# Optimization experiments

Measured on AMD Instinct MI355X. Metric: run time of the kernel, lower is better.

Reference implementation:

```python
import jax, jax.numpy as jnp
import numpy as np

B, C, T, H, W = 8, 512, 8, 32, 32
CI = C // 2  # inter_channels
EPS = 1e-5


def _conv1x1(x, w, b):
    # x: (b, c, t, h, w); w: (o, c); b: (o,)
    return jnp.einsum('bcthw,oc->bothw', x, w) + b[None, :, None, None, None]


def _maxpool2(v):
    # MaxPool3d(kernel=2, stride=2) on (t, h, w)
    b, c, t, h, w = v.shape
    return v.reshape(b, c, t // 2, 2, h // 2, 2, w // 2, 2).max(axis=(3, 5, 7))


def setup_inputs() -> dict:
    key = jax.random.key(0)
    ks = jax.random.split(key, 12)
    s = 0.02
    return {
        'x': jax.random.normal(ks[0], (B, C, T, H, W), dtype=jnp.float32),
        'theta_w': jax.random.normal(ks[1], (CI, C), dtype=jnp.float32) * s,
        'theta_b': jnp.zeros((CI,), dtype=jnp.float32),
        'phi_w': jax.random.normal(ks[2], (CI, C), dtype=jnp.float32) * s,
        'phi_b': jnp.zeros((CI,), dtype=jnp.float32),
        'g_w': jax.random.normal(ks[3], (CI, C), dtype=jnp.float32) * s,
        'g_b': jnp.zeros((CI,), dtype=jnp.float32),
        'wz_w': jax.random.normal(ks[4], (C, CI), dtype=jnp.float32) * s,
        'wz_b': jnp.zeros((C,), dtype=jnp.float32),
        'bn_gamma': jax.random.uniform(ks[5], (C,), dtype=jnp.float32, minval=0.5, maxval=1.5),
        'bn_beta': jax.random.normal(ks[6], (C,), dtype=jnp.float32) * 0.1,
    }


def reference(x, theta_w, theta_b, phi_w, phi_b, g_w, g_b, wz_w, wz_b, bn_gamma, bn_beta):
    b = x.shape[0]
    # projections (1x1x1 convs == channel matmuls)
    theta_x = _conv1x1(x, theta_w, theta_b)            # (b, ci, t, h, w)
    phi_x = _maxpool2(_conv1x1(x, phi_w, phi_b))       # (b, ci, t/2, h/2, w/2)
    g_x = _maxpool2(_conv1x1(x, g_w, g_b))             # (b, ci, t/2, h/2, w/2)

    ci = theta_x.shape[1]
    q = theta_x.reshape(b, ci, -1).transpose(0, 2, 1)  # (b, N, ci)
    k = phi_x.reshape(b, ci, -1)                       # (b, ci, M)
    v = g_x.reshape(b, ci, -1).transpose(0, 2, 1)      # (b, M, ci)

    f = jnp.einsum('bnc,bcm->bnm', q, k)               # (b, N, M)
    attn = jax.nn.softmax(f, axis=-1)                  # embedded_gaussian
    y = jnp.einsum('bnm,bmc->bnc', attn, v)            # (b, N, ci)
    y = y.transpose(0, 2, 1).reshape(b, ci, *x.shape[2:])

    # Wz: 1x1x1 conv + BatchNorm3d (training-mode batch stats, eps=1e-5)
    z = _conv1x1(y, wz_w, wz_b)                        # (b, C, t, h, w)
    mean = z.mean(axis=(0, 2, 3, 4), keepdims=True)
    var = z.var(axis=(0, 2, 3, 4), keepdims=True)
    z = (z - mean) * jax.lax.rsqrt(var + EPS)
    z = z * bn_gamma[None, :, None, None, None] + bn_beta[None, :, None, None, None]
    return z + x
```

## Files before the change

kernel.cpp:

```cpp
#include <hip/hip_runtime.h>
#include <math.h>

typedef unsigned short u16;
typedef __attribute__((ext_vector_type(8))) _Float16 half8;
typedef __attribute__((ext_vector_type(4))) float f32x4;

#define NS 8192
#define MS 1024
#define CCH 512
#define CI 256
#define O3 768

__device__ __forceinline__ float h2f(u16 u) {
    _Float16 h; *(u16*)&h = u; return (float)h;
}
__device__ __forceinline__ u16 f2h(float f) {
    _Float16 h = (_Float16)f; return *(u16*)&h;
}

__device__ __forceinline__ void gld16(u16* lds, const u16* g) {
    __builtin_amdgcn_global_load_lds((const __attribute__((address_space(1))) void*)g,
                                     (__attribute__((address_space(3))) void*)lds,
                                     16, 0, 0);
}

template<int CTRL>
__device__ __forceinline__ float dppmax(float x) {
    union { float f; int i; } a, b;
    a.f = x;
    b.i = __builtin_amdgcn_update_dpp(a.i, a.i, CTRL, 0xF, 0xF, false);
    return fmaxf(a.f, b.f);
}
__device__ __forceinline__ float rowmax16(float x) {
    x = dppmax<0xB1>(x);
    x = dppmax<0x4E>(x);
    x = dppmax<0x141>(x);
    x = dppmax<0x140>(x);
    return x;
}

__global__ void prep_w(const float* __restrict__ tw, const float* __restrict__ tb,
                       const float* __restrict__ pw, const float* __restrict__ pb,
                       const float* __restrict__ gw, const float* __restrict__ gb,
                       const float* __restrict__ wzw,
                       u16* __restrict__ W3b, float* __restrict__ b3, u16* __restrict__ wzb) {
    int i = blockIdx.x * 256 + threadIdx.x;
    if (i < O3 * CCH) {
        int o = i >> 9, c = i & 511;
        float v = (o < 256) ? tw[o * 512 + c] : (o < 512) ? pw[(o - 256) * 512 + c]
                                              : gw[(o - 512) * 512 + c];
        W3b[i] = f2h(v);
    } else {
        int j = i - O3 * CCH;
        if (j < CCH * CI) wzb[j] = f2h(wzw[j]);
    }
    if (i < O3) b3[i] = (i < 256) ? tb[i] : (i < 512) ? pb[i - 256] : gb[i - 512];
}

__global__ __launch_bounds__(256) void transpose_x(const float* __restrict__ x,
                                                   u16* __restrict__ xt) {
    __shared__ float tile[64][129];
    int b = blockIdx.z;
    int n0 = blockIdx.x * 128, c0 = blockIdx.y * 64;
    const float* xb = x + ((size_t)b * CCH + c0) * NS + n0;
    int t = threadIdx.x;
    #pragma unroll
    for (int i = 0; i < 32; ++i) {
        int idx = t + i * 256;
        int c = idx >> 7, n = idx & 127;
        tile[c][n] = xb[(size_t)c * NS + n];
    }
    __syncthreads();
    u16* xo = xt + ((size_t)b * NS + n0) * CCH + c0;
    #pragma unroll
    for (int i = 0; i < 16; ++i) {
        int idx = t + i * 256;
        int cp = idx & 31, n = idx >> 5;
        unsigned lo = f2h(tile[2 * cp][n]);
        unsigned hi = f2h(tile[2 * cp + 1][n]);
        *(unsigned*)(xo + (size_t)n * CCH + 2 * cp) = lo | (hi << 16);
    }
}

__global__ __launch_bounds__(256) void proj_gemm(
        const u16* __restrict__ A, const u16* __restrict__ Bm,
        const float* __restrict__ bias,
        u16* __restrict__ projq, u16* __restrict__ P1) {
    __shared__ u16 As[2][128 * 64];
    __shared__ u16 Bs[2][128 * 64];
    const int t = threadIdx.x;
    const int l = t & 63, w = t >> 6;
    const int wr = w >> 1, wc = w & 1;
    const int fr = l & 15, fq = l >> 4;

    const int nx = gridDim.x, ny = gridDim.y;
    int bid = blockIdx.x + nx * (blockIdx.y + ny * blockIdx.z);
    int cpx = (nx * ny * (int)gridDim.z) >> 3;
    int Wd = (bid & 7) * cpx + (bid >> 3);
    int bx = Wd % nx, rem = Wd / nx;
    int by = rem % ny, bz = rem / ny;

    const u16* gA = A + (size_t)bz * NS * CCH + (size_t)(by * 128) * CCH;
    const u16* gB = Bm + (size_t)(bx * 128) * CCH;

    f32x4 acc[4][4];
    #pragma unroll
    for (int m = 0; m < 4; ++m)
        #pragma unroll
        for (int n = 0; n < 4; ++n) acc[m][n] = (f32x4)0.f;

    #define STAGE_AB(buf, k0)                                                 \
        {                                                                     \
            _Pragma("unroll")                                                 \
            for (int i = 0; i < 4; ++i) {                                     \
                int cd = t + i * 256;                                         \
                int row = cd >> 3;                                            \
                int k8 = ((cd & 7) ^ (row & 7)) * 8;                          \
                int lbase = (cd & ~63) * 8;                                   \
                gld16(&As[buf][lbase], gA + (size_t)row * CCH + (k0) + k8);   \
                gld16(&Bs[buf][lbase], gB + (size_t)row * CCH + (k0) + k8);   \
            }                                                                 \
        }

    const int nk = CCH >> 6;
    STAGE_AB(0, 0);
    STAGE_AB(1, 64);

    for (int mt = 0; mt < nk; ++mt) {
        const int cur = mt & 1;
        if (mt == nk - 1) asm volatile("s_waitcnt vmcnt(0)" ::: "memory");
        else              asm volatile("s_waitcnt vmcnt(8)" ::: "memory");
        __builtin_amdgcn_sched_barrier(0);
        __builtin_amdgcn_s_barrier();

        half8 fa[4][2], fb[4][2];
        #pragma unroll
        for (int m = 0; m < 4; ++m)
            #pragma unroll
            for (int kk = 0; kk < 2; ++kk) {
                int ra = wr * 64 + m * 16 + fr;
                int rb = wc * 64 + m * 16 + fr;
                fa[m][kk] = *(const half8*)&As[cur][ra * 64 + ((((kk << 2) | fq)) ^ (ra & 7)) * 8];
                fb[m][kk] = *(const half8*)&Bs[cur][rb * 64 + ((((kk << 2) | fq)) ^ (rb & 7)) * 8];
            }
        __builtin_amdgcn_s_setprio(1);
        #pragma unroll
        for (int kk = 0; kk < 2; ++kk)
            #pragma unroll
            for (int m = 0; m < 4; ++m)
                #pragma unroll
                for (int n = 0; n < 4; ++n)
                    acc[m][n] = __builtin_amdgcn_mfma_f32_16x16x32_f16(
                        fa[m][kk], fb[n][kk], acc[m][n], 0, 0, 0);
        __builtin_amdgcn_s_setprio(0);

        __builtin_amdgcn_s_barrier();
        if (mt + 2 < nk) STAGE_AB(cur, (mt + 2) * 64);
    }
    #undef STAGE_AB

    const int ccol0 = bx * 128 + wc * 64;
    if (ccol0 < 256) {
        u16* gC = projq + (size_t)bz * NS * 256;
        const int crow0 = by * 128 + wr * 64;
        #pragma unroll
        for (int m = 0; m < 4; ++m)
            #pragma unroll
            for (int n = 0; n < 4; ++n) {
                int col = ccol0 + n * 16 + fr;
                float cb = bias[col];
                #pragma unroll
                for (int j = 0; j < 4; ++j) {
                    int row = crow0 + m * 16 + fq * 4 + j;
                    gC[(size_t)row * 256 + col] = f2h(acc[m][n][j] + cb);
                }
            }
    } else {
        int tt = by >> 3;
        int h2 = ((by & 7) << 1) + wr;
        u16* gP = P1 + ((size_t)bz * 2048 + tt * 256 + h2 * 16) * 512;
        #pragma unroll
        for (int mh = 0; mh < 2; ++mh)
            #pragma unroll
            for (int n = 0; n < 4; ++n) {
                int col = ccol0 + n * 16 + fr;
                float cb = bias[col];
                int c1 = col - 256;
                #pragma unroll
                for (int jj = 0; jj < 2; ++jj) {
                    float mx = fmaxf(
                        fmaxf(acc[mh][n][2 * jj], acc[mh][n][2 * jj + 1]),
                        fmaxf(acc[mh + 2][n][2 * jj], acc[mh + 2][n][2 * jj + 1]));
                    int w2 = mh * 8 + fq * 2 + jj;
                    gP[(size_t)w2 * 512 + c1] = f2h(mx + cb);
                }
            }
    }
}

__global__ __launch_bounds__(256) void pool2_kernel(const u16* __restrict__ P1,
                                                    u16* __restrict__ kb,
                                                    u16* __restrict__ vg) {
    int tid = blockIdx.x * 256 + threadIdx.x;
    int b = tid >> 18;
    int m = (tid >> 8) & 1023;
    int ci = tid & 255;
    int tp = m >> 8, hw = m & 255;
    const u16* p0 = P1 + ((size_t)b * 2048 + (2 * tp) * 256 + hw) * 512;
    const u16* p1 = p0 + 256 * 512;
    float k = fmaxf(h2f(p0[ci]), h2f(p1[ci]));
    float v = fmaxf(h2f(p0[256 + ci]), h2f(p1[256 + ci]));
    kb[((size_t)b * MS + m) * CI + ci] = f2h(k);
    vg[((size_t)b * CI + ci) * MS + m] = f2h(v);
}

template<int BIAS_MODE>
__global__ __launch_bounds__(256) void gemm_nt_f16(
        const u16* __restrict__ A, const u16* __restrict__ Bm,
        u16* __restrict__ C, const float* __restrict__ bias,
        int lda, int ldb, int ldc, int Ksize,
        size_t strideA, size_t strideB, size_t strideC) {
    __shared__ u16 As[2][128 * 64];
    __shared__ u16 Bs[2][128 * 64];
    const int t = threadIdx.x;
    const int l = t & 63, w = t >> 6;
    const int wr = w >> 1, wc = w & 1;
    const int fr = l & 15, fq = l >> 4;

    const int nx = gridDim.x, ny = gridDim.y;
    int bid = blockIdx.x + nx * (blockIdx.y + ny * blockIdx.z);
    int cpx = (nx * ny * (int)gridDim.z) >> 3;
    int Wd = (bid & 7) * cpx + (bid >> 3);
    int bx = Wd % nx, rem = Wd / nx;
    int by = rem % ny, bz = rem / ny;

    const u16* gA = A + (size_t)bz * strideA + (size_t)(by * 128) * lda;
    const u16* gB = Bm + (size_t)bz * strideB + (size_t)(bx * 128) * ldb;

    f32x4 acc[4][4];
    #pragma unroll
    for (int m = 0; m < 4; ++m)
        #pragma unroll
        for (int n = 0; n < 4; ++n) acc[m][n] = (f32x4)0.f;

    #define STAGE_AB(buf, k0)                                                 \
        {                                                                     \
            _Pragma("unroll")                                                 \
            for (int i = 0; i < 4; ++i) {                                     \
                int cd = t + i * 256;                                         \
                int row = cd >> 3;                                            \
                int k8 = ((cd & 7) ^ (row & 7)) * 8;                          \
                int lbase = (cd & ~63) * 8;                                   \
                gld16(&As[buf][lbase], gA + (size_t)row * lda + (k0) + k8);   \
                gld16(&Bs[buf][lbase], gB + (size_t)row * ldb + (k0) + k8);   \
            }                                                                 \
        }

    const int nk = Ksize >> 6;
    STAGE_AB(0, 0);
    STAGE_AB(1, 64);

    for (int mt = 0; mt < nk; ++mt) {
        const int cur = mt & 1;
        if (mt == nk - 1) asm volatile("s_waitcnt vmcnt(0)" ::: "memory");
        else              asm volatile("s_waitcnt vmcnt(8)" ::: "memory");
        __builtin_amdgcn_sched_barrier(0);
        __builtin_amdgcn_s_barrier();

        half8 fa[4][2], fb[4][2];
        #pragma unroll
        for (int m = 0; m < 4; ++m)
            #pragma unroll
            for (int kk = 0; kk < 2; ++kk) {
                int ra = wr * 64 + m * 16 + fr;
                int rb = wc * 64 + m * 16 + fr;
                fa[m][kk] = *(const half8*)&As[cur][ra * 64 + ((((kk << 2) | fq)) ^ (ra & 7)) * 8];
                fb[m][kk] = *(const half8*)&Bs[cur][rb * 64 + ((((kk << 2) | fq)) ^ (rb & 7)) * 8];
            }
        __builtin_amdgcn_s_setprio(1);
        #pragma unroll
        for (int kk = 0; kk < 2; ++kk)
            #pragma unroll
            for (int m = 0; m < 4; ++m)
                #pragma unroll
                for (int n = 0; n < 4; ++n)
                    acc[m][n] = __builtin_amdgcn_mfma_f32_16x16x32_f16(
                        fa[m][kk], fb[n][kk], acc[m][n], 0, 0, 0);
        __builtin_amdgcn_s_setprio(0);

        __builtin_amdgcn_s_barrier();
        if (mt + 2 < nk) STAGE_AB(cur, (mt + 2) * 64);
    }
    #undef STAGE_AB

    u16* gC = C + (size_t)bz * strideC;
    const int crow0 = by * 128 + wr * 64;
    const int ccol0 = bx * 128 + wc * 64;
    #pragma unroll
    for (int m = 0; m < 4; ++m) {
        #pragma unroll
        for (int n = 0; n < 4; ++n) {
            int col = ccol0 + n * 16 + fr;
            float cb = (BIAS_MODE == 2) ? bias[col] : 0.f;
            #pragma unroll
            for (int j = 0; j < 4; ++j) {
                int row = crow0 + m * 16 + fq * 4 + j;
                float v = acc[m][n][j] + cb;
                if (BIAS_MODE == 1) v += bias[row];
                gC[(size_t)row * ldc + col] = f2h(v);
            }
        }
    }
}

__global__ __launch_bounds__(512, 2) void attn_fused(
        const u16* __restrict__ projq, const u16* __restrict__ kb,
        const u16* __restrict__ vg, u16* __restrict__ y) {
    __shared__ u16 Ks[2][64 * 256];
    __shared__ u16 Vs[2][256 * 64];
    __shared__ u16 Ps[8][16][40];

    int bid0 = blockIdx.x + 64 * blockIdx.y;
    int W = (bid0 & 7) * 64 + (bid0 >> 3);
    const int b = W >> 6;
    const int n0 = (W & 63) * 128;

    const int t = threadIdx.x;
    const int l = t & 63, w = t >> 6;
    const int fr = l & 15, fq = l >> 4;

    const u16* projb = projq + (size_t)b * NS * 256;
    const u16* kbb = kb + (size_t)b * MS * CI;
    const u16* vgb = vg + (size_t)b * CI * MS;

    half8 qf[8];
    {
        const u16* qrow = projb + (size_t)(n0 + w * 16 + fr) * 256 + fq * 8;
        #pragma unroll
        for (int kk = 0; kk < 8; ++kk)
            qf[kk] = *(const half8*)(qrow + kk * 32);
    }

    half8 ones;
    #pragma unroll
    for (int i = 0; i < 8; ++i) ones[i] = (_Float16)1.f;

    f32x4 accO[16];
    #pragma unroll
    for (int nf = 0; nf < 16; ++nf) accO[nf] = (f32x4)0.f;
    f32x4 accL = (f32x4)0.f;
    float m_run[4];
    #pragma unroll
    for (int j = 0; j < 4; ++j) m_run[j] = -1e30f;

    #define STAGE_KV(buf, m0)                                                     \
        {                                                                         \
            _Pragma("unroll")                                                     \
            for (int i = 0; i < 4; ++i) {                                         \
                int c = t + i * 512;                                              \
                int lb = (c & ~63) << 3;                                          \
                int krow = c >> 5, kk8 = c & 31;                                  \
                gld16(&Ks[buf][lb],                                               \
                      kbb + (size_t)((m0) + krow) * CI + ((kk8 ^ (krow & 7)) << 3)); \
                int vrow = c >> 3, vk8 = c & 7;                                   \
                gld16(&Vs[buf][lb],                                               \
                      vgb + (size_t)vrow * MS + (m0) + ((vk8 ^ (vrow & 7)) << 3)); \
            }                                                                     \
        }

    STAGE_KV(0, 0);
    STAGE_KV(1, 64);

    for (int mt = 0; mt < 16; ++mt) {
        const int cur = mt & 1;
        if (mt == 15) asm volatile("s_waitcnt vmcnt(0)" ::: "memory");
        else          asm volatile("s_waitcnt vmcnt(8)" ::: "memory");
        __builtin_amdgcn_sched_barrier(0);
        __builtin_amdgcn_s_barrier();

        f32x4 accS[4];
        #pragma unroll
        for (int nf = 0; nf < 4; ++nf) accS[nf] = (f32x4)0.f;
        __builtin_amdgcn_s_setprio(1);
        #pragma unroll
        for (int kk = 0; kk < 8; ++kk) {
            half8 fb[4];
            #pragma unroll
            for (int nf = 0; nf < 4; ++nf) {
                int row = nf * 16 + fr;
                fb[nf] = *(const half8*)&Ks[cur][row * 256 + (((kk << 2) | fq) ^ (row & 7)) * 8];
            }
            #pragma unroll
            for (int nf = 0; nf < 4; ++nf)
                accS[nf] = __builtin_amdgcn_mfma_f32_16x16x32_f16(
                    qf[kk], fb[nf], accS[nf], 0, 0, 0);
        }
        __builtin_amdgcn_s_setprio(0);

        float pm[4];
        #pragma unroll
        for (int j = 0; j < 4; ++j)
            pm[j] = rowmax16(fmaxf(fmaxf(accS[0][j], accS[1][j]),
                                   fmaxf(accS[2][j], accS[3][j])));

        int chg = 0;
        #pragma unroll
        for (int j = 0; j < 4; ++j) chg |= (pm[j] > m_run[j]);
        if (__any(chg)) {
            #pragma unroll
            for (int j = 0; j < 4; ++j) {
                float mn = fmaxf(m_run[j], pm[j]);
                float a = __expf(m_run[j] - mn);
                m_run[j] = mn;
                accL[j] *= a;
                #pragma unroll
                for (int nf = 0; nf < 16; ++nf) accO[nf][j] *= a;
            }
        }

        #pragma unroll
        for (int kkm = 0; kkm < 2; ++kkm) {
            #pragma unroll
            for (int j = 0; j < 4; ++j)
                #pragma unroll
                for (int nfh = 0; nfh < 2; ++nfh) {
                    float p = __expf(accS[kkm * 2 + nfh][j] - m_run[j]);
                    Ps[w][fq * 4 + j][nfh * 16 + fr] = f2h(p);
                }
            half8 fa = *(const half8*)&Ps[w][fr][fq * 8];
            accL = __builtin_amdgcn_mfma_f32_16x16x32_f16(fa, ones, accL, 0, 0, 0);
            __builtin_amdgcn_s_setprio(1);
            #pragma unroll
            for (int nf = 0; nf < 16; ++nf) {
                int row = nf * 16 + fr;
                half8 fbv = *(const half8*)&Vs[cur][row * 64 + (((kkm << 2) | fq) ^ (row & 7)) * 8];
                accO[nf] = __builtin_amdgcn_mfma_f32_16x16x32_f16(
                    fa, fbv, accO[nf], 0, 0, 0);
            }
            __builtin_amdgcn_s_setprio(0);
        }

        __builtin_amdgcn_s_barrier();
        if (mt < 14) STAGE_KV(cur, (mt + 2) * 64);
    }

    u16* yb = y + ((size_t)b * NS + n0 + w * 16) * CI;
    #pragma unroll
    for (int j = 0; j < 4; ++j) {
        float inv = 1.f / accL[j];
        int row = fq * 4 + j;
        #pragma unroll
        for (int nf = 0; nf < 16; ++nf)
            yb[(size_t)row * CI + nf * 16 + fr] = f2h(accO[nf][j] * inv);
    }
    #undef STAGE_KV
}

__global__ __launch_bounds__(256) void bn_stats(const u16* __restrict__ z,
                                                float* __restrict__ stats) {
    int c = blockIdx.x, t = threadIdx.x;
    float s = 0.f, q = 0.f;
    for (int b = 0; b < 8; ++b) {
        const u16* p = z + ((size_t)b * CCH + c) * NS;
        #pragma unroll
        for (int i = 0; i < 4; ++i) {
            uint4 v = *(const uint4*)(p + (t + i * 256) * 8);
            const u16* u = (const u16*)&v;
            #pragma unroll
            for (int j = 0; j < 8; ++j) { float f = h2f(u[j]); s += f; q += f * f; }
        }
    }
    #pragma unroll
    for (int off = 32; off; off >>= 1) { s += __shfl_xor(s, off); q += __shfl_xor(q, off); }
    __shared__ float rs[4], rq[4];
    int w = t >> 6;
    if ((t & 63) == 0) { rs[w] = s; rq[w] = q; }
    __syncthreads();
    if (t == 0) {
        float S2 = rs[0] + rs[1] + rs[2] + rs[3];
        float Q = rq[0] + rq[1] + rq[2] + rq[3];
        const float inv = 1.f / 65536.f;
        float mean = S2 * inv;
        float var = Q * inv - mean * mean;
        stats[c] = mean;
        stats[CCH + c] = rsqrtf(var + 1e-5f);
    }
}

__global__ __launch_bounds__(256) void bn_final(const u16* __restrict__ z,
                                                const float* __restrict__ x,
                                                const float* __restrict__ stats,
                                                const float* __restrict__ gamma,
                                                const float* __restrict__ beta,
                                                float* __restrict__ out) {
    size_t i = ((size_t)blockIdx.x * 256 + threadIdx.x) * 8;
    int c = (int)((i >> 13) & 511);
    float g = gamma[c] * stats[CCH + c];
    float sh = beta[c] - stats[c] * g;
    uint4 zv = *(const uint4*)(z + i);
    const u16* u = (const u16*)&zv;
    float4 x0 = *(const float4*)(x + i);
    float4 x1 = *(const float4*)(x + i + 4);
    float4 o0, o1;
    o0.x = h2f(u[0]) * g + sh + x0.x;
    o0.y = h2f(u[1]) * g + sh + x0.y;
    o0.z = h2f(u[2]) * g + sh + x0.z;
    o0.w = h2f(u[3]) * g + sh + x0.w;
    o1.x = h2f(u[4]) * g + sh + x1.x;
    o1.y = h2f(u[5]) * g + sh + x1.y;
    o1.z = h2f(u[6]) * g + sh + x1.z;
    o1.w = h2f(u[7]) * g + sh + x1.w;
    *(float4*)(out + i) = o0;
    *(float4*)(out + i + 4) = o1;
}

extern "C" void kernel_launch(void* const* d_in, const int* in_sizes, int n_in,
                              void* d_out, int out_size, void* d_ws, size_t ws_size,
                              hipStream_t stream) {
    const float* x       = (const float*)d_in[0];
    const float* theta_w = (const float*)d_in[1];
    const float* theta_b = (const float*)d_in[2];
    const float* phi_w   = (const float*)d_in[3];
    const float* phi_b   = (const float*)d_in[4];
    const float* g_w     = (const float*)d_in[5];
    const float* g_b     = (const float*)d_in[6];
    const float* wz_w    = (const float*)d_in[7];
    const float* wz_b    = (const float*)d_in[8];
    const float* gamma   = (const float*)d_in[9];
    const float* beta    = (const float*)d_in[10];

    char* base = (char*)d_ws;
    u16*   W3b   = (u16*)base;
    float* b3    = (float*)(base + 786432);
    u16*   wzb   = (u16*)(base + 789504);
    float* stats = (float*)(base + 1051648);
    u16*   projq = (u16*)(base + 1056768);
    u16*   P1    = (u16*)(base + 1056768 + 33554432);
    u16*   kb    = (u16*)(base + 1056768 + 50331648);
    u16*   vg    = (u16*)(base + 1056768 + 54525952);
    u16*   xt    = (u16*)(base + 1056768 + 58720256);
    u16*   y     = (u16*)(base + 1056768 + 125829120);
    u16*   z     = (u16*)(base + 1056768 + 159383552);

    prep_w<<<2048, 256, 0, stream>>>(theta_w, theta_b, phi_w, phi_b, g_w, g_b,
                                     wz_w, W3b, b3, wzb);
    transpose_x<<<dim3(64, 8, 8), 256, 0, stream>>>(x, xt);

    proj_gemm<<<dim3(6, 64, 8), 256, 0, stream>>>(xt, W3b, b3, projq, P1);

    pool2_kernel<<<8192, 256, 0, stream>>>(P1, kb, vg);

    attn_fused<<<dim3(64, 8), 512, 0, stream>>>(projq, kb, vg, y);

    gemm_nt_f16<1><<<dim3(64, 4, 8), 256, 0, stream>>>(
        wzb, y, z, wz_b, CI, CI, NS, CI,
        0, (size_t)NS * CI, (size_t)CCH * NS);

    bn_stats<<<CCH, 256, 0, stream>>>(z, stats);

    bn_final<<<16384, 256, 0, stream>>>(z, x, stats, gamma, beta, (float*)d_out);
}
```

Before: 346.2 us.

## Process two query fragments per wave in fused attention to reuse K/V tiles

Each wave of the attention kernel now handles 32 query rows instead of 16. Every K and V fragment loaded from LDS therefore feeds two MFMAs, and each block covers 256 queries, which halves the grid and the total K/V staging traffic. In exchange the accumulator register footprint doubles (accO grows to 128 floats per lane), and the min-blocks-per-CU launch bound is dropped. This risks lower occupancy or spills, and 256 blocks may underfill the CUs.

```diff
diff --git a/kernel.cpp b/kernel.cpp
--- a/kernel.cpp
+++ b/kernel.cpp
@@ -313,17 +313,17 @@
     }
 }
 
-__global__ __launch_bounds__(512, 2) void attn_fused(
+__global__ __launch_bounds__(512) void attn_fused(
         const u16* __restrict__ projq, const u16* __restrict__ kb,
         const u16* __restrict__ vg, u16* __restrict__ y) {
     __shared__ u16 Ks[2][64 * 256];
     __shared__ u16 Vs[2][256 * 64];
-    __shared__ u16 Ps[8][16][40];
-
-    int bid0 = blockIdx.x + 64 * blockIdx.y;
-    int W = (bid0 & 7) * 64 + (bid0 >> 3);
-    const int b = W >> 6;
-    const int n0 = (W & 63) * 128;
+    __shared__ u16 Ps[8][32][40];
+
+    int bid0 = blockIdx.x + 32 * blockIdx.y;
+    int W = (bid0 & 7) * 32 + (bid0 >> 3);
+    const int b = W >> 5;
+    const int n0 = (W & 31) * 256;
 
     const int t = threadIdx.x;
     const int l = t & 63, w = t >> 6;
@@ -333,25 +333,31 @@
     const u16* kbb = kb + (size_t)b * MS * CI;
     const u16* vgb = vg + (size_t)b * CI * MS;
 
-    half8 qf[8];
-    {
-        const u16* qrow = projb + (size_t)(n0 + w * 16 + fr) * 256 + fq * 8;
+    half8 qf[2][8];
+    #pragma unroll
+    for (int mf = 0; mf < 2; ++mf) {
+        const u16* qrow = projb + (size_t)(n0 + w * 32 + mf * 16 + fr) * 256 + fq * 8;
         #pragma unroll
         for (int kk = 0; kk < 8; ++kk)
-            qf[kk] = *(const half8*)(qrow + kk * 32);
+            qf[mf][kk] = *(const half8*)(qrow + kk * 32);
     }
 
     half8 ones;
     #pragma unroll
     for (int i = 0; i < 8; ++i) ones[i] = (_Float16)1.f;
 
-    f32x4 accO[16];
-    #pragma unroll
-    for (int nf = 0; nf < 16; ++nf) accO[nf] = (f32x4)0.f;
-    f32x4 accL = (f32x4)0.f;
-    float m_run[4];
-    #pragma unroll
-    for (int j = 0; j < 4; ++j) m_run[j] = -1e30f;
+    f32x4 accO[2][16];
+    #pragma unroll
+    for (int mf = 0; mf < 2; ++mf)
+        #pragma unroll
+        for (int nf = 0; nf < 16; ++nf) accO[mf][nf] = (f32x4)0.f;
+    f32x4 accL[2];
+    accL[0] = (f32x4)0.f; accL[1] = (f32x4)0.f;
+    float m_run[2][4];
+    #pragma unroll
+    for (int mf = 0; mf < 2; ++mf)
+        #pragma unroll
+        for (int j = 0; j < 4; ++j) m_run[mf][j] = -1e30f;
 
     #define STAGE_KV(buf, m0)                                                     \
         {                                                                         \
@@ -378,9 +384,11 @@
         __builtin_amdgcn_sched_barrier(0);
         __builtin_amdgcn_s_barrier();
 
-        f32x4 accS[4];
-        #pragma unroll
-        for (int nf = 0; nf < 4; ++nf) accS[nf] = (f32x4)0.f;
+        f32x4 accS[2][4];
+        #pragma unroll
+        for (int mf = 0; mf < 2; ++mf)
+            #pragma unroll
+            for (int nf = 0; nf < 4; ++nf) accS[mf][nf] = (f32x4)0.f;
         __builtin_amdgcn_s_setprio(1);
         #pragma unroll
         for (int kk = 0; kk < 8; ++kk) {
@@ -391,51 +399,68 @@
                 fb[nf] = *(const half8*)&Ks[cur][row * 256 + (((kk << 2) | fq) ^ (row & 7)) * 8];
             }
             #pragma unroll
-            for (int nf = 0; nf < 4; ++nf)
-                accS[nf] = __builtin_amdgcn_mfma_f32_16x16x32_f16(
-                    qf[kk], fb[nf], accS[nf], 0, 0, 0);
+            for (int mf = 0; mf < 2; ++mf)
+                #pragma unroll
+                for (int nf = 0; nf < 4; ++nf)
+                    accS[mf][nf] = __builtin_amdgcn_mfma_f32_16x16x32_f16(
+                        qf[mf][kk], fb[nf], accS[mf][nf], 0, 0, 0);
         }
         __builtin_amdgcn_s_setprio(0);
 
-        float pm[4];
-        #pragma unroll
-        for (int j = 0; j < 4; ++j)
-            pm[j] = rowmax16(fmaxf(fmaxf(accS[0][j], accS[1][j]),
-                                   fmaxf(accS[2][j], accS[3][j])));
+        float pm[2][4];
+        #pragma unroll
+        for (int mf = 0; mf < 2; ++mf)
+            #pragma unroll
+            for (int j = 0; j < 4; ++j)
+                pm[mf][j] = rowmax16(fmaxf(fmaxf(accS[mf][0][j], accS[mf][1][j]),
+                                           fmaxf(accS[mf][2][j], accS[mf][3][j])));
 
         int chg = 0;
         #pragma unroll
-        for (int j = 0; j < 4; ++j) chg |= (pm[j] > m_run[j]);
+        for (int mf = 0; mf < 2; ++mf)
+            #pragma unroll
+            for (int j = 0; j < 4; ++j) chg |= (pm[mf][j] > m_run[mf][j]);
         if (__any(chg)) {
             #pragma unroll
-            for (int j = 0; j < 4; ++j) {
-                float mn = fmaxf(m_run[j], pm[j]);
-                float a = __expf(m_run[j] - mn);
-                m_run[j] = mn;
-                accL[j] *= a;
-                #pragma unroll
-                for (int nf = 0; nf < 16; ++nf) accO[nf][j] *= a;
-            }
+            for (int mf = 0; mf < 2; ++mf)
+                #pragma unroll
+                for (int j = 0; j < 4; ++j) {
+                    float mn = fmaxf(m_run[mf][j], pm[mf][j]);
+                    float a = __expf(m_run[mf][j] - mn);
+                    m_run[mf][j] = mn;
+                    accL[mf][j] *= a;
+                    #pragma unroll
+                    for (int nf = 0; nf < 16; ++nf) accO[mf][nf][j] *= a;
+                }
         }
 
         #pragma unroll
         for (int kkm = 0; kkm < 2; ++kkm) {
             #pragma unroll
-            for (int j = 0; j < 4; ++j)
-                #pragma unroll
-                for (int nfh = 0; nfh < 2; ++nfh) {
-                    float p = __expf(accS[kkm * 2 + nfh][j] - m_run[j]);
-                    Ps[w][fq * 4 + j][nfh * 16 + fr] = f2h(p);
-                }
-            half8 fa = *(const half8*)&Ps[w][fr][fq * 8];
-            accL = __builtin_amdgcn_mfma_f32_16x16x32_f16(fa, ones, accL, 0, 0, 0);
+            for (int mf = 0; mf < 2; ++mf)
+                #pragma unroll
+                for (int j = 0; j < 4; ++j)
+                    #pragma unroll
+                    for (int nfh = 0; nfh < 2; ++nfh) {
+                        float p = __expf(accS[mf][kkm * 2 + nfh][j] - m_run[mf][j]);
+                        Ps[w][mf * 16 + fq * 4 + j][nfh * 16 + fr] = f2h(p);
+                    }
+            half8 fa[2];
+            #pragma unroll
+            for (int mf = 0; mf < 2; ++mf) {
+                fa[mf] = *(const half8*)&Ps[w][mf * 16 + fr][fq * 8];
+                accL[mf] = __builtin_amdgcn_mfma_f32_16x16x32_f16(
+                    fa[mf], ones, accL[mf], 0, 0, 0);
+            }
             __builtin_amdgcn_s_setprio(1);
             #pragma unroll
             for (int nf = 0; nf < 16; ++nf) {
                 int row = nf * 16 + fr;
                 half8 fbv = *(const half8*)&Vs[cur][row * 64 + (((kkm << 2) | fq) ^ (row & 7)) * 8];
-                accO[nf] = __builtin_amdgcn_mfma_f32_16x16x32_f16(
-                    fa, fbv, accO[nf], 0, 0, 0);
+                #pragma unroll
+                for (int mf = 0; mf < 2; ++mf)
+                    accO[mf][nf] = __builtin_amdgcn_mfma_f32_16x16x32_f16(
+                        fa[mf], fbv, accO[mf][nf], 0, 0, 0);
             }
             __builtin_amdgcn_s_setprio(0);
         }
@@ -444,15 +469,17 @@
         if (mt < 14) STAGE_KV(cur, (mt + 2) * 64);
     }
 
-    u16* yb = y + ((size_t)b * NS + n0 + w * 16) * CI;
-    #pragma unroll
-    for (int j = 0; j < 4; ++j) {
-        float inv = 1.f / accL[j];
-        int row = fq * 4 + j;
-        #pragma unroll
-        for (int nf = 0; nf < 16; ++nf)
-            yb[(size_t)row * CI + nf * 16 + fr] = f2h(accO[nf][j] * inv);
-    }
+    u16* yb = y + ((size_t)b * NS + n0 + w * 32) * CI;
+    #pragma unroll
+    for (int mf = 0; mf < 2; ++mf)
+        #pragma unroll
+        for (int j = 0; j < 4; ++j) {
+            float inv = 1.f / accL[mf][j];
+            int row = mf * 16 + fq * 4 + j;
+            #pragma unroll
+            for (int nf = 0; nf < 16; ++nf)
+                yb[(size_t)row * CI + nf * 16 + fr] = f2h(accO[mf][nf][j] * inv);
+        }
     #undef STAGE_KV
 }
 
@@ -550,7 +577,7 @@
 
     pool2_kernel<<<8192, 256, 0, stream>>>(P1, kb, vg);
 
-    attn_fused<<<dim3(64, 8), 512, 0, stream>>>(projq, kb, vg, y);
+    attn_fused<<<dim3(32, 8), 512, 0, stream>>>(projq, kb, vg, y);
 
     gemm_nt_f16<1><<<dim3(64, 4, 8), 256, 0, stream>>>(
         wzb, y, z, wz_b, CI, CI, NS, CI,
```

New measurement: 356.2 us. +2.9%, slower.
